# Performance work log

Measured on AMD Instinct MI355X. Metric: run time of the kernel, lower is better.

The kernel has to match this reference:

```python
import jax, jax.numpy as jnp
import numpy as np

TEMPERATURE = 0.07
HARD_NEG_RATIO = 0.5
B, D, N_CLASSES = 2048, 512, 100


def setup_inputs() -> dict:
    key = jax.random.key(0)
    kf, kl = jax.random.split(key)
    features = jax.random.normal(kf, (B, D), dtype=jnp.float32)
    # L2-normalize as is standard for SupCon embeddings (keeps logits well-scaled)
    features = features / jnp.linalg.norm(features, axis=1, keepdims=True)
    labels = jax.random.randint(kl, (B,), 0, N_CLASSES, dtype=jnp.int64)
    return {"features": features, "labels": labels}


def reference(features, labels):
    b = features.shape[0]
    dt = features.dtype
    lab = labels.reshape(-1, 1)
    mask = (lab == lab.T).astype(dt)                       # [B,B] positives (incl. self)
    adc = (features @ features.T) / TEMPERATURE            # [B,B] logits
    logits_max = jax.lax.stop_gradient(jnp.max(adc, axis=1, keepdims=True))
    logits = adc - logits_max                              # row-stabilized
    logits_mask = 1.0 - jnp.eye(b, dtype=dt)               # exclude self
    negative_mask = (1.0 - mask) * logits_mask
    neg_b = negative_mask > 0

    # top-k hard-negative threshold: k-th largest negative logit (global over all pairs).
    # k is data-dependent, so use a full descending sort + dynamic gather (jit-safe).
    flat = jnp.where(neg_b, logits, -jnp.inf).ravel()      # [B*B]
    sorted_desc = -jnp.sort(-flat)
    n_neg = jnp.sum(neg_b)
    k = jnp.maximum(1, (HARD_NEG_RATIO * n_neg).astype(jnp.int32))  # floor, >=1
    threshold = sorted_desc[k - 1]
    hard_negatives_mask = ((logits >= threshold) & neg_b).astype(dt)

    final_mask = jnp.minimum(mask + hard_negatives_mask, 1.0) * logits_mask
    row_pos = final_mask.sum(axis=1)
    single_samples = (row_pos == 0).astype(dt)

    exp_logits = jnp.exp(logits) * logits_mask
    log_prob = logits - jnp.log(exp_logits.sum(axis=1, keepdims=True) + 1e-12)
    mean_log_prob_pos = (final_mask * log_prob).sum(axis=1) / (row_pos + single_samples)
    loss_vec = -mean_log_prob_pos * (1.0 - single_samples)
    loss = loss_vec.sum() / (b - single_samples.sum())
    return (loss, hard_negatives_mask, final_mask)
```

## Files before the change

kernel.cpp:

```cpp
#include <hip/hip_runtime.h>
#include <cstddef>

constexpr int Bn   = 2048;
constexpr int Dn   = 512;
constexpr int NCLS = 100;
constexpr unsigned WWIN = 32768;
constexpr int NH = 32768;


struct Ctl {
  unsigned above;
  unsigned candCount;
  unsigned singles;
  unsigned done;
  float    thrF;
  unsigned pad1;
  double   lossSum;
  unsigned hist[NH];
  unsigned done8[128];
  unsigned sing8[128];
};
static_assert(offsetof(Ctl, hist) == 32, "zero loop covers head + hist + slices");

__device__ inline unsigned key_of(float L) {
  unsigned u = __float_as_uint(L);
  return (u & 0x80000000u) ? ~u : (u | 0x80000000u);
}
__device__ inline float key_to_float(unsigned key) {
  unsigned u = (key & 0x80000000u) ? (key ^ 0x80000000u) : ~key;
  return __uint_as_float(u);
}
__device__ inline unsigned wlo_key() {
  const float c0 = -1.0f / 0.07f;
  return key_of(c0) - (WWIN / 2);
}
__device__ inline void agent_store_f64(double* p, double v) {
  __hip_atomic_store(p, v, __ATOMIC_RELAXED, __HIP_MEMORY_SCOPE_AGENT);
}
__device__ inline void agent_store_u32(unsigned* p, unsigned v) {
  __hip_atomic_store(p, v, __ATOMIC_RELAXED, __HIP_MEMORY_SCOPE_AGENT);
}

__global__ __launch_bounds__(64) void rowdot_k(const float* __restrict__ F,
                                               float* __restrict__ rm, Ctl* c) {
  const int i = blockIdx.x * 64 + threadIdx.x;
  const float4* p = (const float4*)(F + (size_t)i * Dn);
  float acc = 0.0f;
#pragma unroll 16
  for (int q = 0; q < 128; ++q) {
    const float4 f = p[q];
    acc = __builtin_fmaf(f.x, f.x, acc);
    acc = __builtin_fmaf(f.y, f.y, acc);
    acc = __builtin_fmaf(f.z, f.z, acc);
    acc = __builtin_fmaf(f.w, f.w, acc);
  }
  rm[i] = acc / 0.07f;
  unsigned* cz = (unsigned*)c;
  for (int idx = i; idx < 8 + NH + 256; idx += 2048) cz[idx] = 0;
}

__global__ __launch_bounds__(256) void gemm_adc(const float* __restrict__ F,
                                                const float* __restrict__ rm,
                                                const int* __restrict__ labels,
                                                float* __restrict__ adc, Ctl* c) {
  __shared__ float smem[8704];
  __shared__ int slabi[64], slabj[64];
  __shared__ float rmiA[64], rmjA[64];
  __shared__ unsigned abcnt;
  __shared__ unsigned amlast;
  const int t = threadIdx.x;
  int r = 0;
  { const int idx = blockIdx.x; while ((r + 1) * (r + 2) / 2 <= idx) ++r; }
  const int cc = blockIdx.x - r * (r + 1) / 2;
  const int i0 = r * 64, j0 = cc * 64;

  const int tx = t & 15, ty = t >> 4;
  const int lrow = t >> 2, lq = t & 3;

  if (t < 64) {
    slabi[t] = labels[i0 + t]; rmiA[t] = rm[i0 + t];
    slabj[t] = labels[j0 + t]; rmjA[t] = rm[j0 + t];
  }
  if (t == 0) abcnt = 0;

  float acc[4][4] = {};
  const float* Ab = F + (size_t)(i0 + lrow) * Dn;
  const float* Bb = F + (size_t)(j0 + lrow) * Dn;
  float* As = smem;
  float* Bs = smem + 4352;

  float4 a0 = *(const float4*)(Ab + lq * 4);
  float4 a1 = *(const float4*)(Ab + lq * 4 + 16);
  float4 b0 = *(const float4*)(Bb + lq * 4);
  float4 b1 = *(const float4*)(Bb + lq * 4 + 16);
  {
    const int k0 = lq * 4;
    As[(k0 + 0) * 68 + lrow] = a0.x; As[(k0 + 1) * 68 + lrow] = a0.y;
    As[(k0 + 2) * 68 + lrow] = a0.z; As[(k0 + 3) * 68 + lrow] = a0.w;
    As[(k0 + 16) * 68 + lrow] = a1.x; As[(k0 + 17) * 68 + lrow] = a1.y;
    As[(k0 + 18) * 68 + lrow] = a1.z; As[(k0 + 19) * 68 + lrow] = a1.w;
    Bs[(k0 + 0) * 68 + lrow] = b0.x; Bs[(k0 + 1) * 68 + lrow] = b0.y;
    Bs[(k0 + 2) * 68 + lrow] = b0.z; Bs[(k0 + 3) * 68 + lrow] = b0.w;
    Bs[(k0 + 16) * 68 + lrow] = b1.x; Bs[(k0 + 17) * 68 + lrow] = b1.y;
    Bs[(k0 + 18) * 68 + lrow] = b1.z; Bs[(k0 + 19) * 68 + lrow] = b1.w;
  }
  __syncthreads();

  for (int ch = 0; ch < 16; ++ch) {
    const int cur = ch & 1, nxt = cur ^ 1;
    if (ch < 15) {
      const int kg = (ch + 1) * 32;
      a0 = *(const float4*)(Ab + kg + lq * 4);
      a1 = *(const float4*)(Ab + kg + lq * 4 + 16);
      b0 = *(const float4*)(Bb + kg + lq * 4);
      b1 = *(const float4*)(Bb + kg + lq * 4 + 16);
    }
    const float* Ac = As + cur * 2176;
    const float* Bc = Bs + cur * 2176;
#pragma unroll
    for (int k = 0; k < 32; ++k) {
      const float4 av = *(const float4*)(Ac + k * 68 + ty * 4);
      const float4 bv = *(const float4*)(Bc + k * 68 + tx * 4);
      const float aa[4] = {av.x, av.y, av.z, av.w};
      const float bb[4] = {bv.x, bv.y, bv.z, bv.w};
#pragma unroll
      for (int m = 0; m < 4; ++m)
#pragma unroll
        for (int n = 0; n < 4; ++n)
          acc[m][n] = __builtin_fmaf(aa[m], bb[n], acc[m][n]);
    }
    if (ch < 15) {
      const int k0 = lq * 4;
      float* An = As + nxt * 2176;
      float* Bm = Bs + nxt * 2176;
      An[(k0 + 0) * 68 + lrow] = a0.x; An[(k0 + 1) * 68 + lrow] = a0.y;
      An[(k0 + 2) * 68 + lrow] = a0.z; An[(k0 + 3) * 68 + lrow] = a0.w;
      An[(k0 + 16) * 68 + lrow] = a1.x; An[(k0 + 17) * 68 + lrow] = a1.y;
      An[(k0 + 18) * 68 + lrow] = a1.z; An[(k0 + 19) * 68 + lrow] = a1.w;
      Bm[(k0 + 0) * 68 + lrow] = b0.x; Bm[(k0 + 1) * 68 + lrow] = b0.y;
      Bm[(k0 + 2) * 68 + lrow] = b0.z; Bm[(k0 + 3) * 68 + lrow] = b0.w;
      Bm[(k0 + 16) * 68 + lrow] = b1.x; Bm[(k0 + 17) * 68 + lrow] = b1.y;
      Bm[(k0 + 18) * 68 + lrow] = b1.z; Bm[(k0 + 19) * 68 + lrow] = b1.w;
    }
    __syncthreads();
  }

  float v[4][4];
#pragma unroll
  for (int m = 0; m < 4; ++m) {
#pragma unroll
    for (int n = 0; n < 4; ++n) v[m][n] = acc[m][n] / 0.07f;
    float4 q = {v[m][0], v[m][1], v[m][2], v[m][3]};
    *(float4*)&adc[(size_t)(i0 + ty * 4 + m) * Bn + j0 + tx * 4] = q;
  }
  if (r != cc) {
    __syncthreads();
    float* T = smem;
#pragma unroll
    for (int m = 0; m < 4; ++m)
#pragma unroll
      for (int n = 0; n < 4; ++n)
        T[(tx * 4 + n) * 68 + (ty * 4 + m)] = v[m][n];
    __syncthreads();
#pragma unroll
    for (int e = 0; e < 4; ++e) {
      const int row2 = e * 16 + ty;
      *(float4*)&adc[(size_t)(j0 + row2) * Bn + i0 + tx * 4] =
          *(const float4*)(T + row2 * 68 + tx * 4);
    }
  }

  __syncthreads();
  const unsigned klo = wlo_key(), khi = klo + WWIN;
  unsigned myab = 0;
#pragma unroll
  for (int m = 0; m < 4; ++m) {
    const int gi = i0 + ty * 4 + m;
    const int li = slabi[ty * 4 + m];
    const float rmi = rmiA[ty * 4 + m];
#pragma unroll
    for (int n = 0; n < 4; ++n) {
      const int gj = j0 + tx * 4 + n;
      if (gi == gj || li == slabj[tx * 4 + n]) continue;
      const unsigned key = key_of(v[m][n] - rmi);
      if (key >= khi) ++myab;
      else if (key >= klo) atomicAdd(&c->hist[key - klo], 1u);
      if (r != cc) {
        const unsigned key2 = key_of(v[m][n] - rmjA[tx * 4 + n]);
        if (key2 >= khi) ++myab;
        else if (key2 >= klo) atomicAdd(&c->hist[key2 - klo], 1u);
      }
    }
  }
  if (myab) atomicAdd(&abcnt, myab);
  __syncthreads();
  if (t == 0 && abcnt) atomicAdd(&c->above, abcnt);

  __syncthreads();
  if (t == 0) {
    const int sl = (int)(blockIdx.x & 7);
    unsigned am = 0u;
    if (atomicAdd(&c->done8[sl * 16], 1u) == 65u)
      am = (atomicAdd(&c->done, 1u) == 7u) ? 1u : 0u;
    amlast = am;
  }
  __syncthreads();
  if (!amlast) return;

  unsigned* s_cnt  = (unsigned*)smem;
  unsigned* s_tsum = (unsigned*)smem + 128;
  unsigned* s_scan = (unsigned*)smem + 384;
  if (t < 128) s_cnt[t] = 0;
  __syncthreads();
  for (int j = t; j < Bn; j += 256) atomicAdd(&s_cnt[labels[j]], 1u);
  __syncthreads();
  s_scan[t] = (t < NCLS) ? s_cnt[t] * s_cnt[t] : 0u;
  __syncthreads();
#pragma unroll
  for (int off = 128; off > 0; off >>= 1) {
    if (t < off) s_scan[t] += s_scan[t + off];
    __syncthreads();
  }
  unsigned kk = (((unsigned)Bn * Bn) - s_scan[0]) >> 1;
  if (kk < 1u) kk = 1u;
  __syncthreads();

  const uint4* hp = (const uint4*)c->hist;
  unsigned s = 0;
#pragma unroll 8
  for (int bq = 0; bq < 32; ++bq) {
    const uint4 vq = hp[t * 32 + bq];
    s += vq.x + vq.y + vq.z + vq.w;
  }
  s_tsum[t] = s;
  s_scan[t] = s;
  __syncthreads();
#pragma unroll
  for (int off = 1; off < 256; off <<= 1) {
    const unsigned add = (t + off < 256) ? s_scan[t + off] : 0u;
    __syncthreads();
    s_scan[t] += add;
    __syncthreads();
  }
  const unsigned above = c->above;
  unsigned cum = above + s_scan[t] - s_tsum[t];
  int fbin = -1;
#pragma unroll 8
  for (int bq = 31; bq >= 0; --bq) {
    const uint4 vq = hp[t * 32 + bq];
    const unsigned hq[4] = {vq.x, vq.y, vq.z, vq.w};
#pragma unroll
    for (int u = 3; u >= 0; --u) {
      if (cum < kk && cum + hq[u] >= kk) fbin = t * 128 + bq * 4 + u;
      cum += hq[u];
    }
  }
  if (fbin >= 0) c->thrF = key_to_float(klo + (unsigned)fbin);
}

__global__ __launch_bounds__(256) void final_k(const float* __restrict__ adc,
                                               const int* __restrict__ labels,
                                               Ctl* c,
                                               float* __restrict__ out,
                                               double* __restrict__ lsum_g,
                                               unsigned* __restrict__ scnt_g) {
  __shared__ int slab[Bn];
  __shared__ double lsum[4];
  __shared__ unsigned sflag[4];
  __shared__ unsigned amlast;
  const int t = threadIdx.x;
  const int lane = t & 63, w = t >> 6;
#pragma unroll
  for (int e = 0; e < 2; ++e)
    ((int4*)slab)[t + 256 * e] = ((const int4*)labels)[t + 256 * e];
  __syncthreads();
  const float thr = c->thrF;
  float* __restrict__ ohnm = out + 1;
  float* __restrict__ ofin = out + 1 + (size_t)Bn * Bn;

  const int i = blockIdx.x * 4 + w;
  const int li = slab[i];
  const float rm = adc[(size_t)i * Bn + i];
  const float4* rowp = (const float4*)(adc + (size_t)i * Bn);
  const size_t rowb = (size_t)i * Bn;
  float se = 0.0f, sp = 0.0f;
  int pc = 0;
  float carry_h = 0.0f, carry_f = 0.0f;
  float qh3 = 0.0f, qf3 = 0.0f;
#pragma unroll
  for (int q = 0; q < 8; ++q) {
    const int j4 = lane + 64 * q;
    const float4 vv = rowp[j4];
    const int jb = j4 * 4;
    const float vs[4] = {vv.x, vv.y, vv.z, vv.w};
    float qh[4], qf[4];
#pragma unroll
    for (int u = 0; u < 4; ++u) {
      const int j = jb + u;
      const float L = vs[u] - rm;
      const bool offd = (j != i);
      const bool same = (slab[j] == li);
      const bool hnm  = offd && !same && (L >= thr);
      const bool fin  = offd && (same || hnm);
      if (offd) se += __expf(L);
      if (fin)  { sp += L; ++pc; }
      qh[u] = hnm ? 1.0f : 0.0f;
      qf[u] = fin ? 1.0f : 0.0f;
    }
    float uph = __shfl_up(qh[3], 1, 64);
    float upf = __shfl_up(qf[3], 1, 64);
    if (lane == 0) { uph = carry_h; upf = carry_f; }
    if (q == 0 && lane == 0) {
      ohnm[rowb + 0] = qh[0]; ohnm[rowb + 1] = qh[1]; ohnm[rowb + 2] = qh[2];
      ofin[rowb + 0] = qf[0]; ofin[rowb + 1] = qf[1]; ofin[rowb + 2] = qf[2];
    } else {
      const float4 sh = {uph, qh[0], qh[1], qh[2]};
      const float4 sf = {upf, qf[0], qf[1], qf[2]};
      *(float4*)&ohnm[rowb + jb - 1] = sh;
      *(float4*)&ofin[rowb + jb - 1] = sf;
    }
    carry_h = __shfl(qh[3], 63, 64);
    carry_f = __shfl(qf[3], 63, 64);
    qh3 = qh[3]; qf3 = qf[3];
  }
  if (lane == 63) {
    ohnm[rowb + 2047] = qh3;
    ofin[rowb + 2047] = qf3;
  }
  float pcf = (float)pc;
#pragma unroll
  for (int o = 32; o > 0; o >>= 1) {
    se  += __shfl_down(se,  o, 64);
    sp  += __shfl_down(sp,  o, 64);
    pcf += __shfl_down(pcf, o, 64);
  }
  if (lane == 0) {
    const double P = (double)pcf;
    const bool single = (P == 0.0);
    const double mlpp = ((double)sp - P * log((double)se + 1e-12)) / (P + (single ? 1.0 : 0.0));
    lsum[w]  = single ? 0.0 : -mlpp;
    sflag[w] = single ? 1u : 0u;
  }
  __syncthreads();
  if (t == 0) {
    agent_store_f64(&lsum_g[blockIdx.x], lsum[0] + lsum[1] + lsum[2] + lsum[3]);
    agent_store_u32(&scnt_g[blockIdx.x], sflag[0] + sflag[1] + sflag[2] + sflag[3]);
    asm volatile("s_waitcnt vmcnt(0)" ::: "memory");
    const int sl = (int)(blockIdx.x & 7);
    unsigned am = 0u;
    if (atomicAdd(&c->sing8[sl * 16], 1u) == 63u)
      am = (atomicAdd(&c->singles, 1u) == 7u) ? 1u : 0u;
    amlast = am;
  }
  __syncthreads();
  if (!amlast) return;

  double ls = lsum_g[t] + lsum_g[t + 256];
  unsigned sc = scnt_g[t] + scnt_g[t + 256];
#pragma unroll
  for (int o = 32; o > 0; o >>= 1) {
    ls += __shfl_down(ls, o, 64);
    sc += __shfl_down(sc, o, 64);
  }
  if (lane == 0) { lsum[w] = ls; sflag[w] = sc; }
  __syncthreads();
  if (t == 0) {
    const double tot = lsum[0] + lsum[1] + lsum[2] + lsum[3];
    const unsigned sg = sflag[0] + sflag[1] + sflag[2] + sflag[3];
    out[0] = (float)(tot / ((double)Bn - (double)sg));
  }
}

extern "C" void kernel_launch(void* const* d_in, const int* in_sizes, int n_in,
                              void* d_out, int out_size, void* d_ws, size_t ws_size,
                              hipStream_t stream) {
  const float* F      = (const float*)d_in[0];
  const int*   labels = (const int*)d_in[1];
  float* out = (float*)d_out;

  char* ws = (char*)d_ws;
  Ctl*      c      = (Ctl*)ws;
  float*    rm     = (float*)(ws + 786432);
  double*   lsum_g = (double*)(ws + 802816);
  unsigned* scnt_g = (unsigned*)(ws + 806912);
  float*    adc    = (float*)(ws + (1u << 20));

  rowdot_k<<<32, 64, 0, stream>>>(F, rm, c);
  gemm_adc<<<528, 256, 0, stream>>>(F, rm, labels, adc, c);
  final_k<<<512, 256, 0, stream>>>(adc, labels, c, out, lsum_g, scnt_g);
}
```

Before: 150.8 us.

## Enlarge symmetric GEMM tiles to 128x128 with 4x4x4 register blocking

Each block now computes a 128x128 tile of the symmetric Gram matrix, and each thread holds a 2x2 grid of 4x4 accumulators. This cuts the grid from 528 to 136 triangular blocks and raises data reuse per shared-memory load. The transposed write-back is split into four staged passes, and the last-block counter threshold is adjusted to match. The cost is far fewer blocks than CUs and higher register pressure, which may leave much of the GPU idle.

```diff
diff --git a/kernel.cpp b/kernel.cpp
--- a/kernel.cpp
+++ b/kernel.cpp
@@ -63,110 +63,140 @@
                                                 const float* __restrict__ rm,
                                                 const int* __restrict__ labels,
                                                 float* __restrict__ adc, Ctl* c) {
-  __shared__ float smem[8704];
-  __shared__ int slabi[64], slabj[64];
-  __shared__ float rmiA[64], rmjA[64];
+  __shared__ float smem[8448];
+  __shared__ int slabi[128], slabj[128];
+  __shared__ float rmiA[128], rmjA[128];
   __shared__ unsigned abcnt;
   __shared__ unsigned amlast;
   const int t = threadIdx.x;
   int r = 0;
   { const int idx = blockIdx.x; while ((r + 1) * (r + 2) / 2 <= idx) ++r; }
   const int cc = blockIdx.x - r * (r + 1) / 2;
-  const int i0 = r * 64, j0 = cc * 64;
+  const int i0 = r * 128, j0 = cc * 128;
 
   const int tx = t & 15, ty = t >> 4;
-  const int lrow = t >> 2, lq = t & 3;
-
-  if (t < 64) {
+  const int lrow = t >> 1, lkh = (t & 1) * 8;
+
+  if (t < 128) {
     slabi[t] = labels[i0 + t]; rmiA[t] = rm[i0 + t];
     slabj[t] = labels[j0 + t]; rmjA[t] = rm[j0 + t];
   }
   if (t == 0) abcnt = 0;
 
-  float acc[4][4] = {};
-  const float* Ab = F + (size_t)(i0 + lrow) * Dn;
-  const float* Bb = F + (size_t)(j0 + lrow) * Dn;
+  float acc[2][2][4][4] = {};
+  const float* Ab = F + (size_t)(i0 + lrow) * Dn + lkh;
+  const float* Bb = F + (size_t)(j0 + lrow) * Dn + lkh;
   float* As = smem;
-  float* Bs = smem + 4352;
-
-  float4 a0 = *(const float4*)(Ab + lq * 4);
-  float4 a1 = *(const float4*)(Ab + lq * 4 + 16);
-  float4 b0 = *(const float4*)(Bb + lq * 4);
-  float4 b1 = *(const float4*)(Bb + lq * 4 + 16);
+  float* Bs = smem + 4224;
+
+  float4 a0 = *(const float4*)(Ab);
+  float4 a1 = *(const float4*)(Ab + 4);
+  float4 b0 = *(const float4*)(Bb);
+  float4 b1 = *(const float4*)(Bb + 4);
   {
-    const int k0 = lq * 4;
-    As[(k0 + 0) * 68 + lrow] = a0.x; As[(k0 + 1) * 68 + lrow] = a0.y;
-    As[(k0 + 2) * 68 + lrow] = a0.z; As[(k0 + 3) * 68 + lrow] = a0.w;
-    As[(k0 + 16) * 68 + lrow] = a1.x; As[(k0 + 17) * 68 + lrow] = a1.y;
-    As[(k0 + 18) * 68 + lrow] = a1.z; As[(k0 + 19) * 68 + lrow] = a1.w;
-    Bs[(k0 + 0) * 68 + lrow] = b0.x; Bs[(k0 + 1) * 68 + lrow] = b0.y;
-    Bs[(k0 + 2) * 68 + lrow] = b0.z; Bs[(k0 + 3) * 68 + lrow] = b0.w;
-    Bs[(k0 + 16) * 68 + lrow] = b1.x; Bs[(k0 + 17) * 68 + lrow] = b1.y;
-    Bs[(k0 + 18) * 68 + lrow] = b1.z; Bs[(k0 + 19) * 68 + lrow] = b1.w;
-  }
-  __syncthreads();
-
-  for (int ch = 0; ch < 16; ++ch) {
-    const int cur = ch & 1, nxt = cur ^ 1;
-    if (ch < 15) {
-      const int kg = (ch + 1) * 32;
-      a0 = *(const float4*)(Ab + kg + lq * 4);
-      a1 = *(const float4*)(Ab + kg + lq * 4 + 16);
-      b0 = *(const float4*)(Bb + kg + lq * 4);
-      b1 = *(const float4*)(Bb + kg + lq * 4 + 16);
-    }
-    const float* Ac = As + cur * 2176;
-    const float* Bc = Bs + cur * 2176;
-#pragma unroll
-    for (int k = 0; k < 32; ++k) {
-      const float4 av = *(const float4*)(Ac + k * 68 + ty * 4);
-      const float4 bv = *(const float4*)(Bc + k * 68 + tx * 4);
-      const float aa[4] = {av.x, av.y, av.z, av.w};
-      const float bb[4] = {bv.x, bv.y, bv.z, bv.w};
+    const float av[8] = {a0.x, a0.y, a0.z, a0.w, a1.x, a1.y, a1.z, a1.w};
+    const float bv[8] = {b0.x, b0.y, b0.z, b0.w, b1.x, b1.y, b1.z, b1.w};
+#pragma unroll
+    for (int q = 0; q < 8; ++q) {
+      As[(lkh + q) * 132 + lrow] = av[q];
+      Bs[(lkh + q) * 132 + lrow] = bv[q];
+    }
+  }
+  __syncthreads();
+
+  for (int ch2 = 0; ch2 < 32; ++ch2) {
+    const int cur = ch2 & 1, nxt = cur ^ 1;
+    if (ch2 < 31) {
+      const int kg = (ch2 + 1) * 16;
+      a0 = *(const float4*)(Ab + kg);
+      a1 = *(const float4*)(Ab + kg + 4);
+      b0 = *(const float4*)(Bb + kg);
+      b1 = *(const float4*)(Bb + kg + 4);
+    }
+    const float* Ac = As + cur * 2112;
+    const float* Bc = Bs + cur * 2112;
+#pragma unroll
+    for (int k = 0; k < 16; ++k) {
+      const float4 al = *(const float4*)(Ac + k * 132 + ty * 4);
+      const float4 ah = *(const float4*)(Ac + k * 132 + 64 + ty * 4);
+      const float4 bl = *(const float4*)(Bc + k * 132 + tx * 4);
+      const float4 bh = *(const float4*)(Bc + k * 132 + 64 + tx * 4);
+      const float aL[4] = {al.x, al.y, al.z, al.w};
+      const float aH[4] = {ah.x, ah.y, ah.z, ah.w};
+      const float bL[4] = {bl.x, bl.y, bl.z, bl.w};
+      const float bH[4] = {bh.x, bh.y, bh.z, bh.w};
 #pragma unroll
       for (int m = 0; m < 4; ++m)
 #pragma unroll
+        for (int n = 0; n < 4; ++n) {
+          acc[0][0][m][n] = __builtin_fmaf(aL[m], bL[n], acc[0][0][m][n]);
+          acc[0][1][m][n] = __builtin_fmaf(aL[m], bH[n], acc[0][1][m][n]);
+          acc[1][0][m][n] = __builtin_fmaf(aH[m], bL[n], acc[1][0][m][n]);
+          acc[1][1][m][n] = __builtin_fmaf(aH[m], bH[n], acc[1][1][m][n]);
+        }
+    }
+    if (ch2 < 31) {
+      const float av[8] = {a0.x, a0.y, a0.z, a0.w, a1.x, a1.y, a1.z, a1.w};
+      const float bv[8] = {b0.x, b0.y, b0.z, b0.w, b1.x, b1.y, b1.z, b1.w};
+      float* An = As + nxt * 2112;
+      float* Bm = Bs + nxt * 2112;
+#pragma unroll
+      for (int q = 0; q < 8; ++q) {
+        An[(lkh + q) * 132 + lrow] = av[q];
+        Bm[(lkh + q) * 132 + lrow] = bv[q];
+      }
+    }
+    __syncthreads();
+  }
+
+  float v[2][2][4][4];
+#pragma unroll
+  for (int rh = 0; rh < 2; ++rh)
+#pragma unroll
+    for (int chh = 0; chh < 2; ++chh)
+#pragma unroll
+      for (int m = 0; m < 4; ++m)
+#pragma unroll
         for (int n = 0; n < 4; ++n)
-          acc[m][n] = __builtin_fmaf(aa[m], bb[n], acc[m][n]);
-    }
-    if (ch < 15) {
-      const int k0 = lq * 4;
-      float* An = As + nxt * 2176;
-      float* Bm = Bs + nxt * 2176;
-      An[(k0 + 0) * 68 + lrow] = a0.x; An[(k0 + 1) * 68 + lrow] = a0.y;
-      An[(k0 + 2) * 68 + lrow] = a0.z; An[(k0 + 3) * 68 + lrow] = a0.w;
-      An[(k0 + 16) * 68 + lrow] = a1.x; An[(k0 + 17) * 68 + lrow] = a1.y;
-      An[(k0 + 18) * 68 + lrow] = a1.z; An[(k0 + 19) * 68 + lrow] = a1.w;
-      Bm[(k0 + 0) * 68 + lrow] = b0.x; Bm[(k0 + 1) * 68 + lrow] = b0.y;
-      Bm[(k0 + 2) * 68 + lrow] = b0.z; Bm[(k0 + 3) * 68 + lrow] = b0.w;
-      Bm[(k0 + 16) * 68 + lrow] = b1.x; Bm[(k0 + 17) * 68 + lrow] = b1.y;
-      Bm[(k0 + 18) * 68 + lrow] = b1.z; Bm[(k0 + 19) * 68 + lrow] = b1.w;
-    }
-    __syncthreads();
-  }
-
-  float v[4][4];
-#pragma unroll
-  for (int m = 0; m < 4; ++m) {
-#pragma unroll
-    for (int n = 0; n < 4; ++n) v[m][n] = acc[m][n] / 0.07f;
-    float4 q = {v[m][0], v[m][1], v[m][2], v[m][3]};
-    *(float4*)&adc[(size_t)(i0 + ty * 4 + m) * Bn + j0 + tx * 4] = q;
-  }
+          v[rh][chh][m][n] = acc[rh][chh][m][n] / 0.07f;
+
+#pragma unroll
+  for (int rh = 0; rh < 2; ++rh)
+#pragma unroll
+    for (int m = 0; m < 4; ++m) {
+      const size_t rowo = (size_t)(i0 + rh * 64 + ty * 4 + m) * Bn + j0;
+#pragma unroll
+      for (int chh = 0; chh < 2; ++chh) {
+        const float4 q = {v[rh][chh][m][0], v[rh][chh][m][1],
+                          v[rh][chh][m][2], v[rh][chh][m][3]};
+        *(float4*)&adc[rowo + chh * 64 + tx * 4] = q;
+      }
+    }
+
   if (r != cc) {
-    __syncthreads();
     float* T = smem;
 #pragma unroll
-    for (int m = 0; m < 4; ++m)
-#pragma unroll
-      for (int n = 0; n < 4; ++n)
-        T[(tx * 4 + n) * 68 + (ty * 4 + m)] = v[m][n];
-    __syncthreads();
-#pragma unroll
-    for (int e = 0; e < 4; ++e) {
-      const int row2 = e * 16 + ty;
-      *(float4*)&adc[(size_t)(j0 + row2) * Bn + i0 + tx * 4] =
-          *(const float4*)(T + row2 * 68 + tx * 4);
+    for (int g = 0; g < 4; ++g) {
+      __syncthreads();
+      const int rh = g >> 1, half = g & 1;
+      if ((ty >> 3) == half) {
+        const int ic = (ty & 7) * 4;
+#pragma unroll
+        for (int chh = 0; chh < 2; ++chh)
+#pragma unroll
+          for (int n = 0; n < 4; ++n)
+#pragma unroll
+            for (int m = 0; m < 4; ++m)
+              T[(chh * 64 + tx * 4 + n) * 36 + ic + m] = v[rh][chh][m][n];
+      }
+      __syncthreads();
+      const int jj = t >> 1, qq = t & 1;
+#pragma unroll
+      for (int e = 0; e < 4; ++e) {
+        const int loc = qq * 16 + e * 4;
+        *(float4*)&adc[(size_t)(j0 + jj) * Bn + i0 + g * 32 + loc] =
+            *(const float4*)(T + jj * 36 + loc);
+      }
     }
   }
 
@@ -174,24 +204,30 @@
   const unsigned klo = wlo_key(), khi = klo + WWIN;
   unsigned myab = 0;
 #pragma unroll
-  for (int m = 0; m < 4; ++m) {
-    const int gi = i0 + ty * 4 + m;
-    const int li = slabi[ty * 4 + m];
-    const float rmi = rmiA[ty * 4 + m];
-#pragma unroll
-    for (int n = 0; n < 4; ++n) {
-      const int gj = j0 + tx * 4 + n;
-      if (gi == gj || li == slabj[tx * 4 + n]) continue;
-      const unsigned key = key_of(v[m][n] - rmi);
-      if (key >= khi) ++myab;
-      else if (key >= klo) atomicAdd(&c->hist[key - klo], 1u);
-      if (r != cc) {
-        const unsigned key2 = key_of(v[m][n] - rmjA[tx * 4 + n]);
-        if (key2 >= khi) ++myab;
-        else if (key2 >= klo) atomicAdd(&c->hist[key2 - klo], 1u);
-      }
-    }
-  }
+  for (int rh = 0; rh < 2; ++rh)
+#pragma unroll
+    for (int m = 0; m < 4; ++m) {
+      const int ii = rh * 64 + ty * 4 + m;
+      const int gi = i0 + ii;
+      const int li = slabi[ii];
+      const float rmi = rmiA[ii];
+#pragma unroll
+      for (int chh = 0; chh < 2; ++chh)
+#pragma unroll
+        for (int n = 0; n < 4; ++n) {
+          const int jjn = chh * 64 + tx * 4 + n;
+          const int gj = j0 + jjn;
+          if (gi == gj || li == slabj[jjn]) continue;
+          const unsigned key = key_of(v[rh][chh][m][n] - rmi);
+          if (key >= khi) ++myab;
+          else if (key >= klo) atomicAdd(&c->hist[key - klo], 1u);
+          if (r != cc) {
+            const unsigned key2 = key_of(v[rh][chh][m][n] - rmjA[jjn]);
+            if (key2 >= khi) ++myab;
+            else if (key2 >= klo) atomicAdd(&c->hist[key2 - klo], 1u);
+          }
+        }
+    }
   if (myab) atomicAdd(&abcnt, myab);
   __syncthreads();
   if (t == 0 && abcnt) atomicAdd(&c->above, abcnt);
@@ -200,7 +236,7 @@
   if (t == 0) {
     const int sl = (int)(blockIdx.x & 7);
     unsigned am = 0u;
-    if (atomicAdd(&c->done8[sl * 16], 1u) == 65u)
+    if (atomicAdd(&c->done8[sl * 16], 1u) == 16u)
       am = (atomicAdd(&c->done, 1u) == 7u) ? 1u : 0u;
     amlast = am;
   }
@@ -386,6 +422,6 @@
   float*    adc    = (float*)(ws + (1u << 20));
 
   rowdot_k<<<32, 64, 0, stream>>>(F, rm, c);
-  gemm_adc<<<528, 256, 0, stream>>>(F, rm, labels, adc, c);
+  gemm_adc<<<136, 256, 0, stream>>>(F, rm, labels, adc, c);
   final_k<<<512, 256, 0, stream>>>(adc, labels, c, out, lsum_g, scnt_g);
 }
```

Measured after the change: 184.1 us. +22.1%, slower.
